# Kernel optimization log

Hardware: AMD Instinct MI355X
Metric: run time of the kernel (lower is better)

Reference implementation:

```python
import jax, jax.numpy as jnp
import numpy as np

E = 512   # embed_dim == decoder_dim (structurally required by the module)
D = 512
V = 10000
B = 64
S = 32    # encoded caption length; max decode steps T = S - 1


def _lstm_cell(x, h, c, wih, whh, bih, bhh):
    # torch.nn.LSTMCell gate order: i, f, g, o
    gates = x @ wih.T + h @ whh.T + bih + bhh
    i, f, g, o = jnp.split(gates, 4, axis=-1)
    c2 = jax.nn.sigmoid(f) * c + jax.nn.sigmoid(i) * jnp.tanh(g)
    h2 = jax.nn.sigmoid(o) * jnp.tanh(c2)
    return h2, c2


def setup_inputs() -> dict:
    key = jax.random.key(0)
    ks = jax.random.split(key, 16)
    encoder_out = jax.random.normal(ks[0], (B, E), jnp.float32)
    encoded_captions = jax.random.randint(ks[1], (B, S), 0, V)
    # lengths sorted descending (required by the ragged :batch_size_t slicing); force max = S
    lens = np.sort(np.asarray(jax.random.randint(ks[2], (B,), 8, S + 1)))[::-1].copy()
    lens[0] = S
    caption_lengths = jnp.asarray(lens, jnp.int32)
    u = lambda k, sh: jax.random.uniform(k, sh, jnp.float32, -0.1, 0.1)
    return {
        'encoder_out': encoder_out,
        'encoded_captions': encoded_captions,
        'caption_lengths': caption_lengths,
        'embedding': u(ks[3], (V, E)),
        'dec_wih': u(ks[4], (4 * D, 2 * E)),
        'dec_whh': u(ks[5], (4 * D, D)),
        'dec_bih': u(ks[6], (4 * D,)),
        'dec_bhh': u(ks[7], (4 * D,)),
        'w_wih': u(ks[8], (4, E)),
        'w_whh': u(ks[9], (4, 1)),
        'w_bih': u(ks[10], (4,)),
        'w_bhh': u(ks[11], (4,)),
        'init_h_w': u(ks[12], (1, E)),
        'init_h_b': jnp.zeros((1,), jnp.float32),
        'init_c_w': u(ks[13], (1, E)),
        'init_c_b': jnp.zeros((1,), jnp.float32),
        'cls_w': u(ks[14], (V, D)),
        'cls_b': jnp.zeros((V,), jnp.float32),
    }


def reference(encoder_out, encoded_captions, caption_lengths, embedding,
              dec_wih, dec_whh, dec_bih, dec_bhh,
              w_wih, w_whh, w_bih, w_bhh,
              init_h_w, init_h_b, init_c_w, init_c_b,
              cls_w, cls_b):
    dl = caption_lengths - 1                      # decode lengths, [B]
    T = int(np.max(np.asarray(dl)))
    emb = embedding[encoded_captions]             # [B,S,E]
    xs = jnp.moveaxis(emb[:, :T, :], 1, 0)        # [T,B,E]
    wh0 = encoder_out @ init_h_w.T + init_h_b     # [B,1]
    wc0 = encoder_out @ init_c_w.T + init_c_b     # [B,1]

    def step(carry, inp):
        t, x_e = inp
        h, c, wh, wc = carry
        m = (dl > t).astype(x_e.dtype)[:, None]   # [B,1] active-row mask (ragged batch)
        wh2, wc2 = _lstm_cell(encoder_out, wh, wc, w_wih, w_whh, w_bih, w_bhh)
        x = jnp.concatenate([x_e, encoder_out], axis=-1)           # [B,2E]
        h2, c2 = _lstm_cell(x, h, c, dec_wih, dec_whh, dec_bih, dec_bhh)
        preds = (h2 @ cls_w.T + cls_b) * m        # inactive rows stay 0 (dropout is eval-mode identity)
        wgt = jax.nn.sigmoid(wh2)[:, 0] * m[:, 0] # [B]
        keep = m > 0
        carry = (jnp.where(keep, h2, h), jnp.where(keep, c2, c),
                 jnp.where(keep, wh2, wh), jnp.where(keep, wc2, wc))
        return carry, (preds, wgt)

    carry0 = (encoder_out, encoder_out, wh0, wc0)
    _, (p_seq, w_seq) = jax.lax.scan(step, carry0, (jnp.arange(T), xs))
    predictions = jnp.moveaxis(p_seq, 0, 1)                        # [B,T,V]
    weights = jnp.broadcast_to(w_seq.T[:, :, None], (B, T, V))     # replicate per-step scalar across vocab
    return predictions, dl, weights
```

## Files before the change

kernel.cpp:

```cpp
#include <hip/hip_runtime.h>
#include <hip/hip_bf16.h>


typedef __attribute__((ext_vector_type(4))) float f32x4;
typedef __attribute__((ext_vector_type(8))) short short8;
typedef __attribute__((ext_vector_type(4))) unsigned short u16x4;

#define BB 64
#define SS 32
#define TT 31
#define EE 512
#define VV 10000

__device__ __forceinline__ float sigf(float x){ return 1.0f/(1.0f + __expf(-x)); }
__device__ __forceinline__ float tanh_(float x){
  x = fminf(15.f, fmaxf(-15.f, x));
  float e = __expf(2.f*x);
  return (e-1.f)/(e+1.f);
}
__device__ __forceinline__ unsigned short f2bf(float x){
  __hip_bfloat16 h = __float2bfloat16(x);
  return __builtin_bit_cast(unsigned short, h);
}
__device__ __forceinline__ short8 ld16_coh(const void* p){
  short8 r;
  asm volatile("global_load_dwordx4 %0, %1, off sc0 sc1" : "=v"(r) : "v"(p) : "memory");
  return r;
}
__device__ __forceinline__ void st8_coh(void* p, unsigned long long v){
  asm volatile("global_store_dwordx2 %0, %1, off sc0 sc1" :: "v"(p), "v"(v) : "memory");
}

#define NPREP 2048
__global__ __launch_bounds__(256) void k_prep(
    const float* __restrict__ dwih, const float* __restrict__ dwhh,
    const float* __restrict__ emb, const int* __restrict__ cap,
    const float* __restrict__ enc,
    __hip_bfloat16* __restrict__ wihbf, __hip_bfloat16* __restrict__ whhbf,
    __hip_bfloat16* __restrict__ xa, __hip_bfloat16* __restrict__ h0,
    const int* __restrict__ caplen,
    const float* __restrict__ wwih, const float* __restrict__ wwhh,
    const float* __restrict__ wbih, const float* __restrict__ wbhh,
    const float* __restrict__ ihw, const float* __restrict__ ihb,
    const float* __restrict__ icw, const float* __restrict__ icb,
    float* __restrict__ wgt, unsigned* __restrict__ flags,
    float* __restrict__ dl_out)
{
  if (blockIdx.x >= NPREP){
    int b = blockIdx.x - NPREP;
    int w = threadIdx.x >> 6, lane = threadIdx.x & 63;
    __shared__ float sv[6];

    float p = 0.f;
    for (int k = lane; k < EE; k += 64) p += enc[b*EE + k] * wwih[w*EE + k];
    #pragma unroll
    for (int off = 32; off; off >>= 1) p += __shfl_down(p, off, 64);
    if (lane == 0) sv[w] = p;

    if (w < 2){
      const float* iw = (w == 0) ? ihw : icw;
      float q = 0.f;
      for (int k = lane; k < EE; k += 64) q += enc[b*EE + k] * iw[k];
      #pragma unroll
      for (int off = 32; off; off >>= 1) q += __shfl_down(q, off, 64);
      if (lane == 0) sv[4 + w] = q + ((w == 0) ? ihb[0] : icb[0]);
    }
    __syncthreads();

    if (threadIdx.x == 0){
      float wh = sv[4], wc = sv[5];
      int dl = caplen[b] - 1;
      for (int t = 0; t < TT; t++){
        float gi = sv[0] + wh*wwhh[0] + wbih[0] + wbhh[0];
        float gf = sv[1] + wh*wwhh[1] + wbih[1] + wbhh[1];
        float gg = sv[2] + wh*wwhh[2] + wbih[2] + wbhh[2];
        float go = sv[3] + wh*wwhh[3] + wbih[3] + wbhh[3];
        float wc2 = sigf(gf)*wc + sigf(gi)*tanh_(gg);
        float wh2 = sigf(go)*tanh_(wc2);
        float m = (dl > t) ? 1.f : 0.f;
        wgt[b*TT + t] = sigf(wh2) * m;
        if (dl > t){ wh = wh2; wc = wc2; }
      }
      dl_out[b] = (float)dl;
    }
    if (b == 0) for (int i = threadIdx.x; i < 4096; i += 256) flags[i] = 0;
    return;
  }

  const int c1 = 2097152;
  const int c2 = c1 + 1048576;
  const int c3 = c2 + 2031616;
  const int c4 = c3 + 32768;
  for (int i = blockIdx.x*blockDim.x + threadIdx.x; i < c4; i += NPREP*256){
    float v; __hip_bfloat16* dst;
    if (i < c1){ v = dwih[i]; dst = wihbf + i; }
    else if (i < c2){ int j = i - c1; v = dwhh[j]; dst = whhbf + j; }
    else if (i < c3){
      int j = i - c2; int r = j >> 10, k = j & 1023, t = r >> 6, b = r & 63;
      v = (k < 512) ? emb[(size_t)cap[b*SS + t]*EE + k] : enc[b*EE + (k - 512)];
      dst = xa + j;
    } else { int j = i - c3; v = enc[j]; dst = h0 + j; }
    *dst = __float2bfloat16(v);
  }
}

__global__ __launch_bounds__(256) void k_xproj(
    const __hip_bfloat16* __restrict__ xa, const __hip_bfloat16* __restrict__ wihbf,
    const float* __restrict__ bih, const float* __restrict__ bhh,
    float* __restrict__ xp)
{
  int bm = blockIdx.y;
  int bn = blockIdx.x;
  int w = threadIdx.x >> 6, lane = threadIdx.x & 63;
  int col = lane & 15, kg = lane >> 4;
  int m0 = bm*64;
  int n0 = bn*256 + w*64;

  f32x4 acc[4][4] = {};
  for (int kk = 0; kk < 32; kk++){
    short8 a[4], bfr[4];
    #pragma unroll
    for (int i = 0; i < 4; i++){
      a[i]   = *(const short8*)(xa    + (size_t)(m0 + i*16 + col)*1024 + kk*32 + kg*8);
      bfr[i] = *(const short8*)(wihbf + (size_t)(n0 + i*16 + col)*1024 + kk*32 + kg*8);
    }
    #pragma unroll
    for (int mt = 0; mt < 4; mt++)
      #pragma unroll
      for (int nt = 0; nt < 4; nt++)
        acc[mt][nt] = __builtin_amdgcn_mfma_f32_16x16x32_bf16(a[mt], bfr[nt], acc[mt][nt], 0, 0, 0);
  }
  float badd[4]; int ncol[4];
  #pragma unroll
  for (int nt = 0; nt < 4; nt++){ int n = n0 + nt*16 + col; ncol[nt] = n; badd[nt] = bih[n] + bhh[n]; }
  #pragma unroll
  for (int mt = 0; mt < 4; mt++)
    #pragma unroll
    for (int rg = 0; rg < 4; rg++){
      int r = m0 + mt*16 + 4*kg + rg;
      #pragma unroll
      for (int nt = 0; nt < 4; nt++)
        xp[(size_t)r*2048 + ncol[nt]] = acc[mt][nt][rg] + badd[nt];
    }
}

__global__ __launch_bounds__(64, 1) void k_rec(
    const __hip_bfloat16* __restrict__ whhbf,
    const float* __restrict__ xp,
    const float* __restrict__ enc,
    const int* __restrict__ caplen,
    char* __restrict__ hbuf,
    __hip_bfloat16* __restrict__ hout,
    unsigned* __restrict__ flags,
    const float* __restrict__ clsw,
    __hip_bfloat16* __restrict__ clsbf)
{
  const int bid = blockIdx.x;
  const int lane = threadIdx.x;

  if (bid >= 128){
    const int n4 = 1280000;
    for (int i = (bid - 128)*64 + lane; i < n4; i += 384*64){
      f32x4 v = ((const f32x4*)clsw)[i];
      u16x4 o;
      o.x = f2bf(v.x); o.y = f2bf(v.y); o.z = f2bf(v.z); o.w = f2bf(v.w);
      ((u16x4*)clsbf)[i] = o;
    }
    return;
  }

  const int g = bid >> 5, s = bid & 31;
  const int col = lane & 15, kg = lane >> 4;
  const int d0 = s*16;
  const int b  = g*16 + col;
  const int dbase = d0 + 4*kg;

  short8 Aq[4][16];
  #pragma unroll
  for (int q = 0; q < 4; q++){
    const __hip_bfloat16* wrow = whhbf + (size_t)(q*512 + d0 + col)*512;
    #pragma unroll
    for (int kk = 0; kk < 16; kk++)
      Aq[q][kk] = *(const short8*)(wrow + kk*32 + kg*8);
  }
  #pragma unroll
  for (int q = 0; q < 4; q++)
    #pragma unroll
    for (int kk = 0; kk < 16; kk++)
      asm volatile("" : "+v"(Aq[q][kk]));

  float hst[4], cst[4];
  #pragma unroll
  for (int j = 0; j < 4; j++){
    float e = enc[(size_t)b*EE + dbase + j];
    hst[j] = e; cst[j] = e;
  }
  const int dl = caplen[b] - 1;
  unsigned* myflag = flags + (size_t)(g*32 + s)*32;
  const unsigned* pollflag = flags + (size_t)(g*32 + (lane & 31))*32;

  f32x4 xg[4];
  #pragma unroll
  for (int q = 0; q < 4; q++)
    xg[q] = *(const f32x4*)(xp + (size_t)b*2048 + q*512 + dbase);

  for (int t = 0; t < TT; t++){
    if (t > 0){
      const unsigned tgt = (unsigned)t;
      while (1){
        unsigned v = __hip_atomic_load(pollflag, __ATOMIC_RELAXED, __HIP_MEMORY_SCOPE_AGENT);
        v = min(v, (unsigned)__shfl_xor((int)v, 1, 64));
        v = min(v, (unsigned)__shfl_xor((int)v, 2, 64));
        v = min(v, (unsigned)__shfl_xor((int)v, 4, 64));
        v = min(v, (unsigned)__shfl_xor((int)v, 8, 64));
        v = min(v, (unsigned)__shfl_xor((int)v, 16, 64));
        if (v >= tgt) break;
        __builtin_amdgcn_s_sleep(1);
      }
    }

    const char* hc = hbuf + (size_t)(t & 1)*65536 + (size_t)b*1024 + kg*16;
    short8 Bf[16];
    #pragma unroll
    for (int kk = 0; kk < 16; kk++)
      Bf[kk] = ld16_coh(hc + kk*64);

    f32x4 xgn[4];
    if (t + 1 < TT){
      #pragma unroll
      for (int q = 0; q < 4; q++)
        xgn[q] = *(const f32x4*)(xp + (size_t)((t+1)*BB + b)*2048 + q*512 + dbase);
    }

    asm volatile("s_waitcnt vmcnt(0)" ::: "memory");
    __builtin_amdgcn_sched_barrier(0);

    f32x4 acc[4] = {};
    #pragma unroll
    for (int kk = 0; kk < 16; kk++)
      #pragma unroll
      for (int q = 0; q < 4; q++)
        acc[q] = __builtin_amdgcn_mfma_f32_16x16x32_bf16(Aq[q][kk], Bf[kk], acc[q], 0, 0, 0);

    const bool act = dl > t;
    unsigned long long hpack = 0, spack = 0;
    #pragma unroll
    for (int j = 0; j < 4; j++){
      float gi = acc[0][j] + xg[0][j];
      float gf = acc[1][j] + xg[1][j];
      float gg = acc[2][j] + xg[2][j];
      float go = acc[3][j] + xg[3][j];
      float c2 = sigf(gf)*cst[j] + sigf(gi)*tanh_(gg);
      float h2 = sigf(go)*tanh_(c2);
      if (act){ cst[j] = c2; hst[j] = h2; }
      hpack |= (unsigned long long)f2bf(h2)     << (16*j);
      spack |= (unsigned long long)f2bf(hst[j]) << (16*j);
    }

    ((unsigned long long*)hout)[((size_t)b*TT + t)*128 + (dbase >> 2)] = hpack;

    if (t < TT - 1){
      st8_coh(hbuf + (size_t)((t + 1) & 1)*65536 + (size_t)b*1024 + (size_t)dbase*2, spack);
      asm volatile("s_waitcnt vmcnt(0)" ::: "memory");
      if (lane == 0)
        __hip_atomic_store(myflag, (unsigned)(t + 1),
                           __ATOMIC_RELAXED, __HIP_MEMORY_SCOPE_AGENT);
    }

    #pragma unroll
    for (int q = 0; q < 4; q++) xg[q] = xgn[q];
  }
}

__global__ __launch_bounds__(256) void k_cls(
    const __hip_bfloat16* __restrict__ hbf,
    const __hip_bfloat16* __restrict__ wbf,
    const float* __restrict__ clsb,
    const float* __restrict__ wgt,
    float* __restrict__ preds, float* __restrict__ wout)
{
  int bid = blockIdx.x;
  int bn = bid % 79, bm = bid / 79;
  int w = threadIdx.x >> 6, lane = threadIdx.x & 63;
  int col = lane & 15, kg = lane >> 4;
  int m0 = bm*128 + (w >> 1)*64;
  int n0 = bn*128 + (w & 1)*64;
  if (m0 >= 1984) return;

  int arow[4], brow[4];
  #pragma unroll
  for (int i = 0; i < 4; i++){
    arow[i] = min(m0 + i*16 + col, 1983);
    brow[i] = min(n0 + i*16 + col, 9999);
  }
  f32x4 acc[4][4] = {};
  for (int kk = 0; kk < 16; kk++){
    short8 a[4], b[4];
    #pragma unroll
    for (int i = 0; i < 4; i++){
      a[i] = *(const short8*)(hbf + (size_t)arow[i]*512 + kk*32 + kg*8);
      b[i] = *(const short8*)(wbf + (size_t)brow[i]*512 + kk*32 + kg*8);
    }
    #pragma unroll
    for (int mt = 0; mt < 4; mt++)
      #pragma unroll
      for (int nt = 0; nt < 4; nt++)
        acc[mt][nt] = __builtin_amdgcn_mfma_f32_16x16x32_bf16(a[mt], b[nt], acc[mt][nt], 0, 0, 0);
  }
  float cb[4]; int vcol[4]; bool vok[4];
  #pragma unroll
  for (int nt = 0; nt < 4; nt++){
    int v = n0 + nt*16 + col; vcol[nt] = v; vok[nt] = (v < VV);
    cb[nt] = vok[nt] ? clsb[v] : 0.f;
  }
  #pragma unroll
  for (int mt = 0; mt < 4; mt++)
    #pragma unroll
    for (int rg = 0; rg < 4; rg++){
      int r = m0 + mt*16 + 4*kg + rg;
      if (r >= 1984) continue;
      float wv = wgt[r];
      float mf = (wv > 0.f) ? 1.f : 0.f;
      size_t base = (size_t)r*VV;
      #pragma unroll
      for (int nt = 0; nt < 4; nt++){
        if (!vok[nt]) continue;
        preds[base + vcol[nt]] = (acc[mt][nt][rg] + cb[nt]) * mf;
        wout [base + vcol[nt]] = wv;
      }
    }
}

extern "C" void kernel_launch(void* const* d_in, const int* in_sizes, int n_in,
                              void* d_out, int out_size, void* d_ws, size_t ws_size,
                              hipStream_t stream) {
  const float* enc    = (const float*)d_in[0];
  const int*   cap    = (const int*)  d_in[1];
  const int*   caplen = (const int*)  d_in[2];
  const float* emb    = (const float*)d_in[3];
  const float* dwih   = (const float*)d_in[4];
  const float* dwhh   = (const float*)d_in[5];
  const float* dbih   = (const float*)d_in[6];
  const float* dbhh   = (const float*)d_in[7];
  const float* wwih   = (const float*)d_in[8];
  const float* wwhh   = (const float*)d_in[9];
  const float* wbih   = (const float*)d_in[10];
  const float* wbhh   = (const float*)d_in[11];
  const float* ihw    = (const float*)d_in[12];
  const float* ihb    = (const float*)d_in[13];
  const float* icw    = (const float*)d_in[14];
  const float* icb    = (const float*)d_in[15];
  const float* clsw   = (const float*)d_in[16];
  const float* clsb   = (const float*)d_in[17];

  float* preds  = (float*)d_out;
  float* dl_out = preds + (size_t)BB*TT*VV;
  float* wout   = dl_out + BB;

  char* ws = (char*)d_ws;
  float*          wgt   = (float*)         (ws + 0);
  unsigned*       flags = (unsigned*)      (ws + 8192);
  __hip_bfloat16* clsbf = (__hip_bfloat16*)(ws + 24576);
  __hip_bfloat16* wihbf = (__hip_bfloat16*)(ws + 10264576);
  __hip_bfloat16* whhbf = (__hip_bfloat16*)(ws + 14458880);
  __hip_bfloat16* xa    = (__hip_bfloat16*)(ws + 16556032);
  float*          xp    = (float*)         (ws + 20619264);
  char*           hbuf  = (char*)          (ws + 36872192);
  __hip_bfloat16* hout  = (__hip_bfloat16*)(ws + 37003264);

  k_prep <<<NPREP + BB, 256, 0, stream>>>(dwih, dwhh, emb, cap, enc,
                                          wihbf, whhbf, xa,
                                          (__hip_bfloat16*)hbuf,
                                          caplen, wwih, wwhh, wbih, wbhh,
                                          ihw, ihb, icw, icb, wgt, flags, dl_out);
  k_xproj<<<dim3(8, 31), 256, 0, stream>>>(xa, wihbf, dbih, dbhh, xp);
  k_rec  <<<512, 64, 0, stream>>>(whhbf, xp, enc, caplen, hbuf, hout, flags,
                                  clsw, clsbf);
  k_cls  <<<16*79, 256, 0, stream>>>(hout, clsbf, clsb, wgt, preds, wout);
}
```

Baseline: 288.8 us.

## Replace per-block flag barrier with tagged data entries in recurrent exchange

The recurrent kernel no longer publishes hidden state and then sets a separate per-block flag after a store fence. Each 8-byte hidden chunk is now written together with a step tag in a single 16-byte store, and consumers spin until every tag they need matches the current step. This removes the store-wait-flag round trip and the flag polling from the critical path of each timestep. The cost is a doubled exchange buffer, 32 tag loads per poll iteration, and two loads per data fragment where there used to be one. Correctness depends on the 16-byte store landing atomically.

```diff
diff --git a/kernel.cpp b/kernel.cpp
--- a/kernel.cpp
+++ b/kernel.cpp
@@ -5,6 +5,7 @@
 typedef __attribute__((ext_vector_type(4))) float f32x4;
 typedef __attribute__((ext_vector_type(8))) short short8;
 typedef __attribute__((ext_vector_type(4))) unsigned short u16x4;
+typedef __attribute__((ext_vector_type(4))) unsigned u32x4;
 
 #define BB 64
 #define SS 32
@@ -22,14 +23,21 @@
   __hip_bfloat16 h = __float2bfloat16(x);
   return __builtin_bit_cast(unsigned short, h);
 }
-__device__ __forceinline__ short8 ld16_coh(const void* p){
-  short8 r;
-  asm volatile("global_load_dwordx4 %0, %1, off sc0 sc1" : "=v"(r) : "v"(p) : "memory");
+__device__ __forceinline__ unsigned ld_tag(const void* p){
+  unsigned r;
+  asm volatile("global_load_dword %0, %1, off sc0 sc1" : "=v"(r) : "v"(p) : "memory");
   return r;
 }
-__device__ __forceinline__ void st8_coh(void* p, unsigned long long v){
-  asm volatile("global_store_dwordx2 %0, %1, off sc0 sc1" :: "v"(p), "v"(v) : "memory");
-}
+__device__ __forceinline__ unsigned long long ld_dat(const void* p){
+  unsigned long long r;
+  asm volatile("global_load_dwordx2 %0, %1, off sc0 sc1" : "=v"(r) : "v"(p) : "memory");
+  return r;
+}
+__device__ __forceinline__ void st_ent(void* p, unsigned long long data, unsigned tag){
+  u32x4 q; q.x = (unsigned)data; q.y = (unsigned)(data >> 32); q.z = tag; q.w = tag;
+  asm volatile("global_store_dwordx4 %0, %1, off sc0 sc1" :: "v"(p), "v"(q) : "memory");
+}
+
 
 #define NPREP 2048
 __global__ __launch_bounds__(256) void k_prep(
@@ -37,14 +45,13 @@
     const float* __restrict__ emb, const int* __restrict__ cap,
     const float* __restrict__ enc,
     __hip_bfloat16* __restrict__ wihbf, __hip_bfloat16* __restrict__ whhbf,
-    __hip_bfloat16* __restrict__ xa, __hip_bfloat16* __restrict__ h0,
+    __hip_bfloat16* __restrict__ xa, char* __restrict__ exb,
     const int* __restrict__ caplen,
     const float* __restrict__ wwih, const float* __restrict__ wwhh,
     const float* __restrict__ wbih, const float* __restrict__ wbhh,
     const float* __restrict__ ihw, const float* __restrict__ ihb,
     const float* __restrict__ icw, const float* __restrict__ icb,
-    float* __restrict__ wgt, unsigned* __restrict__ flags,
-    float* __restrict__ dl_out)
+    float* __restrict__ wgt, float* __restrict__ dl_out)
 {
   if (blockIdx.x >= NPREP){
     int b = blockIdx.x - NPREP;
@@ -83,7 +90,6 @@
       }
       dl_out[b] = (float)dl;
     }
-    if (b == 0) for (int i = threadIdx.x; i < 4096; i += 256) flags[i] = 0;
     return;
   }
 
@@ -91,16 +97,23 @@
   const int c2 = c1 + 1048576;
   const int c3 = c2 + 2031616;
   const int c4 = c3 + 32768;
-  for (int i = blockIdx.x*blockDim.x + threadIdx.x; i < c4; i += NPREP*256){
-    float v; __hip_bfloat16* dst;
-    if (i < c1){ v = dwih[i]; dst = wihbf + i; }
-    else if (i < c2){ int j = i - c1; v = dwhh[j]; dst = whhbf + j; }
+  const int c5 = c4 + 16384;
+  for (int i = blockIdx.x*blockDim.x + threadIdx.x; i < c5; i += NPREP*256){
+    if (i < c1){ wihbf[i] = __float2bfloat16(dwih[i]); }
+    else if (i < c2){ int j = i - c1; whhbf[j] = __float2bfloat16(dwhh[j]); }
     else if (i < c3){
       int j = i - c2; int r = j >> 10, k = j & 1023, t = r >> 6, b = r & 63;
-      v = (k < 512) ? emb[(size_t)cap[b*SS + t]*EE + k] : enc[b*EE + (k - 512)];
-      dst = xa + j;
-    } else { int j = i - c3; v = enc[j]; dst = h0 + j; }
-    *dst = __float2bfloat16(v);
+      float v = (k < 512) ? emb[(size_t)cap[b*SS + t]*EE + k] : enc[b*EE + (k - 512)];
+      xa[j] = __float2bfloat16(v);
+    } else if (i < c4){
+      int j = i - c3; int b = j >> 9, d = j & 511;
+      *(unsigned short*)(exb + (size_t)b*2048 + (d >> 2)*16 + (d & 3)*2)
+          = f2bf(enc[b*EE + d]);
+    } else {
+      int e = i - c4; int buf = e >> 13, idx = e & 8191;
+      *(unsigned*)(exb + (size_t)buf*131072 + (size_t)idx*16 + 8)
+          = buf ? 0xFFFFFFFFu : 0u;
+    }
   }
 }
 
@@ -149,9 +162,8 @@
     const float* __restrict__ xp,
     const float* __restrict__ enc,
     const int* __restrict__ caplen,
-    char* __restrict__ hbuf,
+    char* __restrict__ ex,
     __hip_bfloat16* __restrict__ hout,
-    unsigned* __restrict__ flags,
     const float* __restrict__ clsw,
     __hip_bfloat16* __restrict__ clsbf)
 {
@@ -174,6 +186,7 @@
   const int d0 = s*16;
   const int b  = g*16 + col;
   const int dbase = d0 + 4*kg;
+  const int pme = (dbase >> 2);
 
   short8 Aq[4][16];
   #pragma unroll
@@ -196,8 +209,6 @@
     hst[j] = e; cst[j] = e;
   }
   const int dl = caplen[b] - 1;
-  unsigned* myflag = flags + (size_t)(g*32 + s)*32;
-  const unsigned* pollflag = flags + (size_t)(g*32 + (lane & 31))*32;
 
   f32x4 xg[4];
   #pragma unroll
@@ -205,25 +216,34 @@
     xg[q] = *(const f32x4*)(xp + (size_t)b*2048 + q*512 + dbase);
 
   for (int t = 0; t < TT; t++){
-    if (t > 0){
-      const unsigned tgt = (unsigned)t;
+    const char* rbase = ex + (size_t)(t & 1)*131072 + (size_t)b*2048;
+
+    {
+      const unsigned tagv = (unsigned)t;
       while (1){
-        unsigned v = __hip_atomic_load(pollflag, __ATOMIC_RELAXED, __HIP_MEMORY_SCOPE_AGENT);
-        v = min(v, (unsigned)__shfl_xor((int)v, 1, 64));
-        v = min(v, (unsigned)__shfl_xor((int)v, 2, 64));
-        v = min(v, (unsigned)__shfl_xor((int)v, 4, 64));
-        v = min(v, (unsigned)__shfl_xor((int)v, 8, 64));
-        v = min(v, (unsigned)__shfl_xor((int)v, 16, 64));
-        if (v >= tgt) break;
-        __builtin_amdgcn_s_sleep(1);
+        unsigned tg[32];
+        #pragma unroll
+        for (int kk = 0; kk < 16; kk++){
+          int p0 = kk*8 + kg*2;
+          tg[2*kk]   = ld_tag(rbase + (size_t)p0*16 + 8);
+          tg[2*kk+1] = ld_tag(rbase + (size_t)(p0 + 1)*16 + 8);
+        }
+        asm volatile("s_waitcnt vmcnt(0)" ::: "memory");
+        __builtin_amdgcn_sched_barrier(0);
+        unsigned bad = 0;
+        #pragma unroll
+        for (int i = 0; i < 32; i++) bad |= (tg[i] ^ tagv);
+        if (__all(bad == 0)) break;
       }
     }
 
-    const char* hc = hbuf + (size_t)(t & 1)*65536 + (size_t)b*1024 + kg*16;
-    short8 Bf[16];
-    #pragma unroll
-    for (int kk = 0; kk < 16; kk++)
-      Bf[kk] = ld16_coh(hc + kk*64);
+    unsigned long long dat[32];
+    #pragma unroll
+    for (int kk = 0; kk < 16; kk++){
+      int p0 = kk*8 + kg*2;
+      dat[2*kk]   = ld_dat(rbase + (size_t)p0*16);
+      dat[2*kk+1] = ld_dat(rbase + (size_t)(p0 + 1)*16);
+    }
 
     f32x4 xgn[4];
     if (t + 1 < TT){
@@ -237,10 +257,13 @@
 
     f32x4 acc[4] = {};
     #pragma unroll
-    for (int kk = 0; kk < 16; kk++)
+    for (int kk = 0; kk < 16; kk++){
+      union { unsigned long long u[2]; short8 v; } pk;
+      pk.u[0] = dat[2*kk]; pk.u[1] = dat[2*kk+1];
       #pragma unroll
       for (int q = 0; q < 4; q++)
-        acc[q] = __builtin_amdgcn_mfma_f32_16x16x32_bf16(Aq[q][kk], Bf[kk], acc[q], 0, 0, 0);
+        acc[q] = __builtin_amdgcn_mfma_f32_16x16x32_bf16(Aq[q][kk], pk.v, acc[q], 0, 0, 0);
+    }
 
     const bool act = dl > t;
     unsigned long long hpack = 0, spack = 0;
@@ -257,14 +280,11 @@
       spack |= (unsigned long long)f2bf(hst[j]) << (16*j);
     }
 
-    ((unsigned long long*)hout)[((size_t)b*TT + t)*128 + (dbase >> 2)] = hpack;
+    ((unsigned long long*)hout)[((size_t)b*TT + t)*128 + pme] = hpack;
 
     if (t < TT - 1){
-      st8_coh(hbuf + (size_t)((t + 1) & 1)*65536 + (size_t)b*1024 + (size_t)dbase*2, spack);
-      asm volatile("s_waitcnt vmcnt(0)" ::: "memory");
-      if (lane == 0)
-        __hip_atomic_store(myflag, (unsigned)(t + 1),
-                           __ATOMIC_RELAXED, __HIP_MEMORY_SCOPE_AGENT);
+      st_ent(ex + (size_t)((t + 1) & 1)*131072 + (size_t)b*2048 + (size_t)pme*16,
+             spack, (unsigned)(t + 1));
     }
 
     #pragma unroll
@@ -359,22 +379,20 @@
 
   char* ws = (char*)d_ws;
   float*          wgt   = (float*)         (ws + 0);
-  unsigned*       flags = (unsigned*)      (ws + 8192);
-  __hip_bfloat16* clsbf = (__hip_bfloat16*)(ws + 24576);
-  __hip_bfloat16* wihbf = (__hip_bfloat16*)(ws + 10264576);
-  __hip_bfloat16* whhbf = (__hip_bfloat16*)(ws + 14458880);
-  __hip_bfloat16* xa    = (__hip_bfloat16*)(ws + 16556032);
-  float*          xp    = (float*)         (ws + 20619264);
-  char*           hbuf  = (char*)          (ws + 36872192);
-  __hip_bfloat16* hout  = (__hip_bfloat16*)(ws + 37003264);
+  char*           ex    = (char*)          (ws + 8192);
+  __hip_bfloat16* clsbf = (__hip_bfloat16*)(ws + 270336);
+  __hip_bfloat16* wihbf = (__hip_bfloat16*)(ws + 10510336);
+  __hip_bfloat16* whhbf = (__hip_bfloat16*)(ws + 14704640);
+  __hip_bfloat16* xa    = (__hip_bfloat16*)(ws + 16801792);
+  float*          xp    = (float*)         (ws + 20865024);
+  __hip_bfloat16* hout  = (__hip_bfloat16*)(ws + 37117952);
 
   k_prep <<<NPREP + BB, 256, 0, stream>>>(dwih, dwhh, emb, cap, enc,
-                                          wihbf, whhbf, xa,
-                                          (__hip_bfloat16*)hbuf,
+                                          wihbf, whhbf, xa, ex,
                                           caplen, wwih, wwhh, wbih, wbhh,
-                                          ihw, ihb, icw, icb, wgt, flags, dl_out);
+                                          ihw, ihb, icw, icb, wgt, dl_out);
   k_xproj<<<dim3(8, 31), 256, 0, stream>>>(xa, wihbf, dbih, dbhh, xp);
-  k_rec  <<<512, 64, 0, stream>>>(whhbf, xp, enc, caplen, hbuf, hout, flags,
+  k_rec  <<<512, 64, 0, stream>>>(whhbf, xp, enc, caplen, ex, hout,
                                   clsw, clsbf);
   k_cls  <<<16*79, 256, 0, stream>>>(hout, clsbf, clsb, wgt, preds, wout);
 }
```

After: 348.3 us. 20.6% more time.

## Fuse classifier GEMM into recurrent kernel, overlapping per-step output projection

Applied to the files above, without the earlier changes.

Merges the separate classifier kernel into the recurrent kernel. The 384 spare blocks poll the per-step flags and compute each timestep's vocabulary projection tile as soon as that step's hidden states are published. The classifier weights are converted from fp32 to bf16 on the fly instead of in a separate pass. Hidden outputs are stored time-major with coherent stores, and flags are now published every step. This overlaps the large output GEMM and its writes with the serial recurrence and removes one launch. In exchange, the fp32 weights are re-read and re-converted for every tile, the classifier work runs in 64-thread blocks, and the spin-waiting blocks compete with the recurrence.

```diff
diff --git a/kernel.cpp b/kernel.cpp
--- a/kernel.cpp
+++ b/kernel.cpp
@@ -4,13 +4,13 @@
 
 typedef __attribute__((ext_vector_type(4))) float f32x4;
 typedef __attribute__((ext_vector_type(8))) short short8;
-typedef __attribute__((ext_vector_type(4))) unsigned short u16x4;
 
 #define BB 64
 #define SS 32
 #define TT 31
 #define EE 512
 #define VV 10000
+#define NTILE 157
 
 __device__ __forceinline__ float sigf(float x){ return 1.0f/(1.0f + __expf(-x)); }
 __device__ __forceinline__ float tanh_(float x){
@@ -144,7 +144,7 @@
     }
 }
 
-__global__ __launch_bounds__(64, 1) void k_rec(
+__global__ __launch_bounds__(64, 1) void k_mega(
     const __hip_bfloat16* __restrict__ whhbf,
     const float* __restrict__ xp,
     const float* __restrict__ enc,
@@ -153,27 +153,99 @@
     __hip_bfloat16* __restrict__ hout,
     unsigned* __restrict__ flags,
     const float* __restrict__ clsw,
-    __hip_bfloat16* __restrict__ clsbf)
+    const float* __restrict__ clsb,
+    const float* __restrict__ wgt,
+    float* __restrict__ preds, float* __restrict__ wout)
 {
   const int bid = blockIdx.x;
   const int lane = threadIdx.x;
+  const int col = lane & 15, kg = lane >> 4;
 
   if (bid >= 128){
-    const int n4 = 1280000;
-    for (int i = (bid - 128)*64 + lane; i < n4; i += 384*64){
-      f32x4 v = ((const f32x4*)clsw)[i];
-      u16x4 o;
-      o.x = f2bf(v.x); o.y = f2bf(v.y); o.z = f2bf(v.z); o.w = f2bf(v.w);
-      ((u16x4*)clsbf)[i] = o;
+    const int cw = bid - 128;
+    for (int tau = cw; tau < TT*NTILE; tau += 384){
+      int mt = tau / NTILE, nt = tau - mt*NTILE;
+
+      {
+        const unsigned tgt = (unsigned)(mt + 1);
+        while (1){
+          unsigned v0 = __hip_atomic_load(flags + (size_t)lane*32,
+                                          __ATOMIC_RELAXED, __HIP_MEMORY_SCOPE_AGENT);
+          unsigned v1 = __hip_atomic_load(flags + (size_t)(lane + 64)*32,
+                                          __ATOMIC_RELAXED, __HIP_MEMORY_SCOPE_AGENT);
+          unsigned v = min(v0, v1);
+          v = min(v, (unsigned)__shfl_xor((int)v, 1, 64));
+          v = min(v, (unsigned)__shfl_xor((int)v, 2, 64));
+          v = min(v, (unsigned)__shfl_xor((int)v, 4, 64));
+          v = min(v, (unsigned)__shfl_xor((int)v, 8, 64));
+          v = min(v, (unsigned)__shfl_xor((int)v, 16, 64));
+          v = min(v, (unsigned)__shfl_xor((int)v, 32, 64));
+          if (v >= tgt) break;
+          __builtin_amdgcn_s_sleep(2);
+        }
+        asm volatile("" ::: "memory");
+      }
+
+      int brow[4]; int vcol[4]; bool vok[4]; float cb[4];
+      #pragma unroll
+      for (int i = 0; i < 4; i++) brow[i] = min(nt*64 + i*16 + col, VV - 1);
+      #pragma unroll
+      for (int ni = 0; ni < 4; ni++){
+        int v = nt*64 + ni*16 + col; vcol[ni] = v; vok[ni] = (v < VV);
+        cb[ni] = vok[ni] ? clsb[v] : 0.f;
+      }
+
+      const __hip_bfloat16* hbase = hout + (size_t)(mt*64)*512;
+      f32x4 acc[4][4] = {};
+      for (int kk = 0; kk < 16; kk++){
+        short8 a[4], bfr[4];
+        #pragma unroll
+        for (int i = 0; i < 4; i++)
+          a[i] = *(const short8*)(hbase + (size_t)(i*16 + col)*512 + kk*32 + kg*8);
+        #pragma unroll
+        for (int i = 0; i < 4; i++){
+          const float* wr = clsw + (size_t)brow[i]*512 + kk*32 + kg*8;
+          f32x4 w0 = *(const f32x4*)wr;
+          f32x4 w1 = *(const f32x4*)(wr + 4);
+          short8 t8;
+          t8[0] = (short)f2bf(w0.x); t8[1] = (short)f2bf(w0.y);
+          t8[2] = (short)f2bf(w0.z); t8[3] = (short)f2bf(w0.w);
+          t8[4] = (short)f2bf(w1.x); t8[5] = (short)f2bf(w1.y);
+          t8[6] = (short)f2bf(w1.z); t8[7] = (short)f2bf(w1.w);
+          bfr[i] = t8;
+        }
+        #pragma unroll
+        for (int mi = 0; mi < 4; mi++)
+          #pragma unroll
+          for (int ni = 0; ni < 4; ni++)
+            acc[mi][ni] = __builtin_amdgcn_mfma_f32_16x16x32_bf16(a[mi], bfr[ni], acc[mi][ni], 0, 0, 0);
+      }
+
+      #pragma unroll
+      for (int mi = 0; mi < 4; mi++)
+        #pragma unroll
+        for (int rg = 0; rg < 4; rg++){
+          int bidx = mi*16 + 4*kg + rg;
+          int r_out = bidx*TT + mt;
+          float wv = wgt[r_out];
+          float mf = (wv > 0.f) ? 1.f : 0.f;
+          size_t obase = (size_t)r_out*VV;
+          #pragma unroll
+          for (int ni = 0; ni < 4; ni++){
+            if (!vok[ni]) continue;
+            preds[obase + vcol[ni]] = (acc[mi][ni][rg] + cb[ni]) * mf;
+            wout [obase + vcol[ni]] = wv;
+          }
+        }
     }
     return;
   }
 
   const int g = bid >> 5, s = bid & 31;
-  const int col = lane & 15, kg = lane >> 4;
   const int d0 = s*16;
   const int b  = g*16 + col;
   const int dbase = d0 + 4*kg;
+  const int pme = (dbase >> 2);
 
   short8 Aq[4][16];
   #pragma unroll
@@ -192,8 +264,8 @@
   float hst[4], cst[4];
   #pragma unroll
   for (int j = 0; j < 4; j++){
-    float e = enc[(size_t)b*EE + dbase + j];
-    hst[j] = e; cst[j] = e;
+    float e0 = enc[(size_t)b*EE + dbase + j];
+    hst[j] = e0; cst[j] = e0;
   }
   const int dl = caplen[b] - 1;
   unsigned* myflag = flags + (size_t)(g*32 + s)*32;
@@ -257,78 +329,20 @@
       spack |= (unsigned long long)f2bf(hst[j]) << (16*j);
     }
 
-    ((unsigned long long*)hout)[((size_t)b*TT + t)*128 + (dbase >> 2)] = hpack;
-
-    if (t < TT - 1){
+    if (t < TT - 1)
       st8_coh(hbuf + (size_t)((t + 1) & 1)*65536 + (size_t)b*1024 + (size_t)dbase*2, spack);
-      asm volatile("s_waitcnt vmcnt(0)" ::: "memory");
-      if (lane == 0)
-        __hip_atomic_store(myflag, (unsigned)(t + 1),
-                           __ATOMIC_RELAXED, __HIP_MEMORY_SCOPE_AGENT);
-    }
-
-    #pragma unroll
-    for (int q = 0; q < 4; q++) xg[q] = xgn[q];
-  }
-}
-
-__global__ __launch_bounds__(256) void k_cls(
-    const __hip_bfloat16* __restrict__ hbf,
-    const __hip_bfloat16* __restrict__ wbf,
-    const float* __restrict__ clsb,
-    const float* __restrict__ wgt,
-    float* __restrict__ preds, float* __restrict__ wout)
-{
-  int bid = blockIdx.x;
-  int bn = bid % 79, bm = bid / 79;
-  int w = threadIdx.x >> 6, lane = threadIdx.x & 63;
-  int col = lane & 15, kg = lane >> 4;
-  int m0 = bm*128 + (w >> 1)*64;
-  int n0 = bn*128 + (w & 1)*64;
-  if (m0 >= 1984) return;
-
-  int arow[4], brow[4];
-  #pragma unroll
-  for (int i = 0; i < 4; i++){
-    arow[i] = min(m0 + i*16 + col, 1983);
-    brow[i] = min(n0 + i*16 + col, 9999);
-  }
-  f32x4 acc[4][4] = {};
-  for (int kk = 0; kk < 16; kk++){
-    short8 a[4], b[4];
-    #pragma unroll
-    for (int i = 0; i < 4; i++){
-      a[i] = *(const short8*)(hbf + (size_t)arow[i]*512 + kk*32 + kg*8);
-      b[i] = *(const short8*)(wbf + (size_t)brow[i]*512 + kk*32 + kg*8);
-    }
-    #pragma unroll
-    for (int mt = 0; mt < 4; mt++)
-      #pragma unroll
-      for (int nt = 0; nt < 4; nt++)
-        acc[mt][nt] = __builtin_amdgcn_mfma_f32_16x16x32_bf16(a[mt], b[nt], acc[mt][nt], 0, 0, 0);
-  }
-  float cb[4]; int vcol[4]; bool vok[4];
-  #pragma unroll
-  for (int nt = 0; nt < 4; nt++){
-    int v = n0 + nt*16 + col; vcol[nt] = v; vok[nt] = (v < VV);
-    cb[nt] = vok[nt] ? clsb[v] : 0.f;
-  }
-  #pragma unroll
-  for (int mt = 0; mt < 4; mt++)
-    #pragma unroll
-    for (int rg = 0; rg < 4; rg++){
-      int r = m0 + mt*16 + 4*kg + rg;
-      if (r >= 1984) continue;
-      float wv = wgt[r];
-      float mf = (wv > 0.f) ? 1.f : 0.f;
-      size_t base = (size_t)r*VV;
-      #pragma unroll
-      for (int nt = 0; nt < 4; nt++){
-        if (!vok[nt]) continue;
-        preds[base + vcol[nt]] = (acc[mt][nt][rg] + cb[nt]) * mf;
-        wout [base + vcol[nt]] = wv;
-      }
-    }
+    st8_coh((unsigned long long*)hout + ((size_t)t*BB + b)*128 + pme, hpack);
+
+    asm volatile("s_waitcnt vmcnt(0)" ::: "memory");
+    if (lane == 0)
+      __hip_atomic_store(myflag, (unsigned)(t + 1),
+                         __ATOMIC_RELAXED, __HIP_MEMORY_SCOPE_AGENT);
+
+    if (t + 1 < TT){
+      #pragma unroll
+      for (int q = 0; q < 4; q++) xg[q] = xgn[q];
+    }
+  }
 }
 
 extern "C" void kernel_launch(void* const* d_in, const int* in_sizes, int n_in,
@@ -360,13 +374,12 @@
   char* ws = (char*)d_ws;
   float*          wgt   = (float*)         (ws + 0);
   unsigned*       flags = (unsigned*)      (ws + 8192);
-  __hip_bfloat16* clsbf = (__hip_bfloat16*)(ws + 24576);
-  __hip_bfloat16* wihbf = (__hip_bfloat16*)(ws + 10264576);
-  __hip_bfloat16* whhbf = (__hip_bfloat16*)(ws + 14458880);
-  __hip_bfloat16* xa    = (__hip_bfloat16*)(ws + 16556032);
-  float*          xp    = (float*)         (ws + 20619264);
-  char*           hbuf  = (char*)          (ws + 36872192);
-  __hip_bfloat16* hout  = (__hip_bfloat16*)(ws + 37003264);
+  __hip_bfloat16* wihbf = (__hip_bfloat16*)(ws + 24576);
+  __hip_bfloat16* whhbf = (__hip_bfloat16*)(ws + 4218880);
+  __hip_bfloat16* xa    = (__hip_bfloat16*)(ws + 6316032);
+  float*          xp    = (float*)         (ws + 10379264);
+  char*           hbuf  = (char*)          (ws + 26632192);
+  __hip_bfloat16* hout  = (__hip_bfloat16*)(ws + 26763264);
 
   k_prep <<<NPREP + BB, 256, 0, stream>>>(dwih, dwhh, emb, cap, enc,
                                           wihbf, whhbf, xa,
@@ -374,7 +387,6 @@
                                           caplen, wwih, wwhh, wbih, wbhh,
                                           ihw, ihb, icw, icb, wgt, flags, dl_out);
   k_xproj<<<dim3(8, 31), 256, 0, stream>>>(xa, wihbf, dbih, dbhh, xp);
-  k_rec  <<<512, 64, 0, stream>>>(whhbf, xp, enc, caplen, hbuf, hout, flags,
-                                  clsw, clsbf);
-  k_cls  <<<16*79, 256, 0, stream>>>(hout, clsbf, clsb, wgt, preds, wout);
-}
+  k_mega <<<512, 64, 0, stream>>>(whhbf, xp, enc, caplen, hbuf, hout, flags,
+                                  clsw, clsb, wgt, preds, wout);
+}
```

New measurement: 348.6 us. 1.21x slower.

## Vectorize prep conversion and swap MFMA operands for 16-byte output stores

Applied to the files above, without the earlier changes.

The prep kernel now converts eight floats per thread with two 16-byte loads and one 16-byte bf16 store, instead of one scalar element per thread. In the x-projection and classifier GEMMs the MFMA operands are swapped so each lane's accumulator holds four consecutive output columns. This lets bias loads and the prediction and weight output stores be 16-byte vector writes instead of scattered 4-byte ones. The classifier writes two large float outputs (predictions and weights), so it is the main target for better store coalescing.

```diff
diff --git a/kernel.cpp b/kernel.cpp
--- a/kernel.cpp
+++ b/kernel.cpp
@@ -21,6 +21,14 @@
 __device__ __forceinline__ unsigned short f2bf(float x){
   __hip_bfloat16 h = __float2bfloat16(x);
   return __builtin_bit_cast(unsigned short, h);
+}
+__device__ __forceinline__ short8 cvt8(f32x4 a, f32x4 b){
+  short8 t;
+  t[0] = (short)f2bf(a.x); t[1] = (short)f2bf(a.y);
+  t[2] = (short)f2bf(a.z); t[3] = (short)f2bf(a.w);
+  t[4] = (short)f2bf(b.x); t[5] = (short)f2bf(b.y);
+  t[6] = (short)f2bf(b.z); t[7] = (short)f2bf(b.w);
+  return t;
 }
 __device__ __forceinline__ short8 ld16_coh(const void* p){
   short8 r;
@@ -87,20 +95,27 @@
     return;
   }
 
-  const int c1 = 2097152;
-  const int c2 = c1 + 1048576;
-  const int c3 = c2 + 2031616;
-  const int c4 = c3 + 32768;
-  for (int i = blockIdx.x*blockDim.x + threadIdx.x; i < c4; i += NPREP*256){
-    float v; __hip_bfloat16* dst;
-    if (i < c1){ v = dwih[i]; dst = wihbf + i; }
-    else if (i < c2){ int j = i - c1; v = dwhh[j]; dst = whhbf + j; }
-    else if (i < c3){
-      int j = i - c2; int r = j >> 10, k = j & 1023, t = r >> 6, b = r & 63;
-      v = (k < 512) ? emb[(size_t)cap[b*SS + t]*EE + k] : enc[b*EE + (k - 512)];
-      dst = xa + j;
-    } else { int j = i - c3; v = enc[j]; dst = h0 + j; }
-    *dst = __float2bfloat16(v);
+  const int n1 = 262144;
+  const int n2 = n1 + 131072;
+  const int n3 = n2 + 253952;
+  const int n4 = n3 + 4096;
+  for (int i = blockIdx.x*blockDim.x + threadIdx.x; i < n4; i += NPREP*256){
+    const float* src; __hip_bfloat16* dst;
+    if (i < n1){ src = dwih + (size_t)i*8; dst = wihbf + (size_t)i*8; }
+    else if (i < n2){ int j = i - n1; src = dwhh + (size_t)j*8; dst = whhbf + (size_t)j*8; }
+    else if (i < n3){
+      int j = i - n2; int e = j*8;
+      int r = e >> 10, k = e & 1023, t = r >> 6, b = r & 63;
+      src = (k < 512) ? emb + (size_t)cap[b*SS + t]*EE + k
+                      : enc + (size_t)b*EE + (k - 512);
+      dst = xa + (size_t)e;
+    } else {
+      int j = i - n3; int e = j*8;
+      src = enc + (size_t)e; dst = h0 + (size_t)e;
+    }
+    f32x4 lo = *(const f32x4*)src;
+    f32x4 hi = *(const f32x4*)(src + 4);
+    *(short8*)dst = cvt8(lo, hi);
   }
 }
 
@@ -118,30 +133,30 @@
 
   f32x4 acc[4][4] = {};
   for (int kk = 0; kk < 32; kk++){
-    short8 a[4], bfr[4];
+    short8 aW[4], aX[4];
     #pragma unroll
     for (int i = 0; i < 4; i++){
-      a[i]   = *(const short8*)(xa    + (size_t)(m0 + i*16 + col)*1024 + kk*32 + kg*8);
-      bfr[i] = *(const short8*)(wihbf + (size_t)(n0 + i*16 + col)*1024 + kk*32 + kg*8);
-    }
-    #pragma unroll
-    for (int mt = 0; mt < 4; mt++)
-      #pragma unroll
-      for (int nt = 0; nt < 4; nt++)
-        acc[mt][nt] = __builtin_amdgcn_mfma_f32_16x16x32_bf16(a[mt], bfr[nt], acc[mt][nt], 0, 0, 0);
-  }
-  float badd[4]; int ncol[4];
-  #pragma unroll
-  for (int nt = 0; nt < 4; nt++){ int n = n0 + nt*16 + col; ncol[nt] = n; badd[nt] = bih[n] + bhh[n]; }
-  #pragma unroll
-  for (int mt = 0; mt < 4; mt++)
-    #pragma unroll
-    for (int rg = 0; rg < 4; rg++){
-      int r = m0 + mt*16 + 4*kg + rg;
-      #pragma unroll
-      for (int nt = 0; nt < 4; nt++)
-        xp[(size_t)r*2048 + ncol[nt]] = acc[mt][nt][rg] + badd[nt];
-    }
+      aW[i] = *(const short8*)(wihbf + (size_t)(n0 + i*16 + col)*1024 + kk*32 + kg*8);
+      aX[i] = *(const short8*)(xa    + (size_t)(m0 + i*16 + col)*1024 + kk*32 + kg*8);
+    }
+    #pragma unroll
+    for (int nt = 0; nt < 4; nt++)
+      #pragma unroll
+      for (int mt = 0; mt < 4; mt++)
+        acc[nt][mt] = __builtin_amdgcn_mfma_f32_16x16x32_bf16(aW[nt], aX[mt], acc[nt][mt], 0, 0, 0);
+  }
+  #pragma unroll
+  for (int nt = 0; nt < 4; nt++){
+    int n = n0 + nt*16 + 4*kg;
+    f32x4 badd = *(const f32x4*)(bih + n);
+    f32x4 b2   = *(const f32x4*)(bhh + n);
+    badd = badd + b2;
+    #pragma unroll
+    for (int mt = 0; mt < 4; mt++){
+      int r = m0 + mt*16 + col;
+      *(f32x4*)(xp + (size_t)r*2048 + n) = acc[nt][mt] + badd;
+    }
+  }
 }
 
 __global__ __launch_bounds__(64, 1) void k_rec(
@@ -174,6 +189,7 @@
   const int d0 = s*16;
   const int b  = g*16 + col;
   const int dbase = d0 + 4*kg;
+  const int pme = (dbase >> 2);
 
   short8 Aq[4][16];
   #pragma unroll
@@ -192,8 +208,8 @@
   float hst[4], cst[4];
   #pragma unroll
   for (int j = 0; j < 4; j++){
-    float e = enc[(size_t)b*EE + dbase + j];
-    hst[j] = e; cst[j] = e;
+    float e0 = enc[(size_t)b*EE + dbase + j];
+    hst[j] = e0; cst[j] = e0;
   }
   const int dl = caplen[b] - 1;
   unsigned* myflag = flags + (size_t)(g*32 + s)*32;
@@ -257,7 +273,7 @@
       spack |= (unsigned long long)f2bf(hst[j]) << (16*j);
     }
 
-    ((unsigned long long*)hout)[((size_t)b*TT + t)*128 + (dbase >> 2)] = hpack;
+    ((unsigned long long*)hout)[((size_t)b*TT + t)*128 + pme] = hpack;
 
     if (t < TT - 1){
       st8_coh(hbuf + (size_t)((t + 1) & 1)*65536 + (size_t)b*1024 + (size_t)dbase*2, spack);
@@ -283,52 +299,48 @@
   int bn = bid % 79, bm = bid / 79;
   int w = threadIdx.x >> 6, lane = threadIdx.x & 63;
   int col = lane & 15, kg = lane >> 4;
-  int m0 = bm*128 + (w >> 1)*64;
-  int n0 = bn*128 + (w & 1)*64;
-  if (m0 >= 1984) return;
-
-  int arow[4], brow[4];
+  int r0 = bm*128 + (w >> 1)*64;
+  int v0 = bn*128 + (w & 1)*64;
+  if (r0 >= 1984) return;
+
+  int vrow[4], rrow[4];
   #pragma unroll
   for (int i = 0; i < 4; i++){
-    arow[i] = min(m0 + i*16 + col, 1983);
-    brow[i] = min(n0 + i*16 + col, 9999);
+    vrow[i] = min(v0 + i*16 + col, VV - 1);
+    rrow[i] = min(r0 + i*16 + col, 1983);
   }
   f32x4 acc[4][4] = {};
   for (int kk = 0; kk < 16; kk++){
     short8 a[4], b[4];
     #pragma unroll
     for (int i = 0; i < 4; i++){
-      a[i] = *(const short8*)(hbf + (size_t)arow[i]*512 + kk*32 + kg*8);
-      b[i] = *(const short8*)(wbf + (size_t)brow[i]*512 + kk*32 + kg*8);
-    }
-    #pragma unroll
-    for (int mt = 0; mt < 4; mt++)
-      #pragma unroll
-      for (int nt = 0; nt < 4; nt++)
-        acc[mt][nt] = __builtin_amdgcn_mfma_f32_16x16x32_bf16(a[mt], b[nt], acc[mt][nt], 0, 0, 0);
-  }
-  float cb[4]; int vcol[4]; bool vok[4];
-  #pragma unroll
-  for (int nt = 0; nt < 4; nt++){
-    int v = n0 + nt*16 + col; vcol[nt] = v; vok[nt] = (v < VV);
-    cb[nt] = vok[nt] ? clsb[v] : 0.f;
-  }
-  #pragma unroll
-  for (int mt = 0; mt < 4; mt++)
-    #pragma unroll
-    for (int rg = 0; rg < 4; rg++){
-      int r = m0 + mt*16 + 4*kg + rg;
+      a[i] = *(const short8*)(wbf + (size_t)vrow[i]*512 + kk*32 + kg*8);
+      b[i] = *(const short8*)(hbf + (size_t)rrow[i]*512 + kk*32 + kg*8);
+    }
+    #pragma unroll
+    for (int vt = 0; vt < 4; vt++)
+      #pragma unroll
+      for (int rt = 0; rt < 4; rt++)
+        acc[vt][rt] = __builtin_amdgcn_mfma_f32_16x16x32_bf16(a[vt], b[rt], acc[vt][rt], 0, 0, 0);
+  }
+
+  #pragma unroll
+  for (int vt = 0; vt < 4; vt++){
+    int v = v0 + vt*16 + 4*kg;
+    if (v >= VV) continue;
+    f32x4 cb4 = *(const f32x4*)(clsb + v);
+    #pragma unroll
+    for (int rt = 0; rt < 4; rt++){
+      int r = r0 + rt*16 + col;
       if (r >= 1984) continue;
       float wv = wgt[r];
       float mf = (wv > 0.f) ? 1.f : 0.f;
-      size_t base = (size_t)r*VV;
-      #pragma unroll
-      for (int nt = 0; nt < 4; nt++){
-        if (!vok[nt]) continue;
-        preds[base + vcol[nt]] = (acc[mt][nt][rg] + cb[nt]) * mf;
-        wout [base + vcol[nt]] = wv;
-      }
-    }
+      f32x4 o = (acc[vt][rt] + cb4) * mf;
+      f32x4 wq = {wv, wv, wv, wv};
+      *(f32x4*)(preds + (size_t)r*VV + v) = o;
+      *(f32x4*)(wout  + (size_t)r*VV + v) = wq;
+    }
+  }
 }
 
 extern "C" void kernel_launch(void* const* d_in, const int* in_sizes, int n_in,
```

Measured after the change: 292.3 us. About the same (+1.2%).
